# Optimization experiments

Measured on AMD Instinct MI355X. Metric: run time of the kernel, lower is better.

The kernel has to match this reference:

```python
import jax, jax.numpy as jnp
import numpy as np
from jax import lax

B, T, F = 8, 512, 128          # batch, mel time, mel freq
DM, DS, DC, EXP, NL = 384, 16, 4, 2, 12
DI = EXP * DM                   # 768 inner width
DTR = (DM + 15) // 16           # 24, mamba_ssm dt_rank='auto'
PT = PF = 16
L = (T // PT) * (F // PF)       # 256 patches
NC = 4


def setup_inputs() -> dict:
    key = jax.random.key(0)
    ks = iter(jax.random.split(key, 24))
    def n(shape, s=0.02):
        return jax.random.normal(next(ks), shape, jnp.float32) * s
    return {
        "x": jax.random.normal(next(ks), (B, T, F), jnp.float32),
        "patch_w": n((DM, PT, PF)),
        "patch_b": jnp.zeros((DM,), jnp.float32),
        "pos_embed": n((1, L, DM)),
        "ln_g": jnp.ones((NL, DM), jnp.float32),
        "ln_b": jnp.zeros((NL, DM), jnp.float32),
        "in_proj_w": n((NL, 2 * DI, DM)),
        "conv_w": n((NL, DI, DC), 0.1),
        "conv_b": jnp.zeros((NL, DI), jnp.float32),
        "x_proj_w": n((NL, DTR + 2 * DS, DI)),
        "dt_proj_w": n((NL, DI, DTR), 0.1),
        "dt_proj_b": n((NL, DI), 0.1),
        "A_log": jnp.tile(jnp.log(jnp.arange(1, DS + 1, dtype=jnp.float32))[None, None, :], (NL, DI, 1)),
        "Dskip": jnp.ones((NL, DI), jnp.float32),
        "out_proj_w": n((NL, DM, DI)),
        "fn_g": jnp.ones((DM,), jnp.float32),
        "fn_b": jnp.zeros((DM,), jnp.float32),
        "head_w": n((NC, DM)),
        "head_b": jnp.zeros((NC,), jnp.float32),
    }


def _layernorm(x, g, b):
    m = x.mean(-1, keepdims=True)
    v = jnp.var(x, axis=-1, keepdims=True)
    return (x - m) * lax.rsqrt(v + 1e-5) * g + b


def _silu(v):
    return v * jax.nn.sigmoid(v)


def _mamba_block(x, p):
    # x: [B, L, DM]; residual Mamba block (pre-LN, dropout=identity in eval)
    ln_g, ln_b, Wi, cw, cb, Wx, Wdt, bdt, A_log, Dsk, Wo = p
    res = x
    h = _layernorm(x, ln_g, ln_b)
    xz = jnp.einsum('bld,ed->ble', h, Wi)          # [B,L,2*DI]
    u, z = jnp.split(xz, 2, axis=-1)
    # causal depthwise conv1d, kernel DC (small, unrolled)
    up = jnp.pad(u, ((0, 0), (DC - 1, 0), (0, 0)))
    u = sum(up[:, k:k + L, :] * cw[:, k] for k in range(DC)) + cb
    u = _silu(u)
    proj = jnp.einsum('bld,ed->ble', u, Wx)        # [B,L,DTR+2*DS]
    dt, Bm, Cm = jnp.split(proj, [DTR, DTR + DS], axis=-1)
    delta = jax.nn.softplus(jnp.einsum('blr,dr->bld', dt, Wdt) + bdt)  # [B,L,DI]
    A = -jnp.exp(A_log)                            # [DI, DS]
    dA = jnp.exp(delta[..., None] * A)             # [B,L,DI,DS]
    dBu = (delta * u)[..., None] * Bm[:, :, None, :]

    def step(hst, inp):
        dA_t, dBu_t, C_t = inp
        hst = dA_t * hst + dBu_t                   # [B,DI,DS]
        return hst, jnp.einsum('bdn,bn->bd', hst, C_t)

    h0 = jnp.zeros((x.shape[0], DI, DS), x.dtype)
    _, ys = lax.scan(step, h0, (dA.swapaxes(0, 1), dBu.swapaxes(0, 1), Cm.swapaxes(0, 1)))
    y = ys.swapaxes(0, 1) + u * Dsk                # [B,L,DI]
    y = y * _silu(z)
    return res + jnp.einsum('bld,ed->ble', y, Wo)


def reference(x, patch_w, patch_b, pos_embed, ln_g, ln_b, in_proj_w, conv_w, conv_b,
              x_proj_w, dt_proj_w, dt_proj_b, A_log, Dskip, out_proj_w,
              fn_g, fn_b, head_w, head_b):
    Bn = x.shape[0]
    # patch embed = non-overlapping 16x16 conv == blocked reshape + einsum
    patches = x.reshape(Bn, T // PT, PT, F // PF, PF)
    tok = jnp.einsum('bhpwq,dpq->bhwd', patches, patch_w) + patch_b
    tok = tok.reshape(Bn, L, DM) + pos_embed

    def layer(carry, p):
        return _mamba_block(carry, p), None

    tok, _ = lax.scan(layer, tok, (ln_g, ln_b, in_proj_w, conv_w, conv_b,
                                   x_proj_w, dt_proj_w, dt_proj_b, A_log, Dskip, out_proj_w))
    tok = _layernorm(tok, fn_g, fn_b)
    pooled = tok.mean(axis=1)
    return pooled @ head_w.T + head_b
```

## Files before the change

### kernel.cpp

```cpp
#include <hip/hip_runtime.h>
#include <math.h>

namespace {

constexpr int kB   = 8;
constexpr int kL   = 256;
constexpr int kTok = 2048;
constexpr int kDM  = 384;
constexpr int kDI  = 768;
constexpr int kDS  = 16;
constexpr int kDTR = 24;
constexpr int kPROJ = 56;
constexpr int kNL  = 12;

constexpr int kWIN  = 2 * kDI * kDM;
constexpr int kWOUT = kDM * kDI;
constexpr int kWX   = kPROJ * kDI;
constexpr int kWTOT = kWIN + kWOUT + kWX;

typedef float f32x4 __attribute__((ext_vector_type(4)));
typedef short short8 __attribute__((ext_vector_type(8)));

__device__ __forceinline__ float softplus_f(float x) {
  return (x > 20.f) ? x : log1pf(__expf(x));
}
__device__ __forceinline__ float silu_f(float x) {
  return x / (1.f + __expf(-x));
}
__device__ __forceinline__ unsigned short f2bf(float f) {
  union { float f; unsigned u; } v; v.f = f;
  unsigned r = v.u + 0x7FFFu + ((v.u >> 16) & 1u);
  return (unsigned short)(r >> 16);
}

__global__ __launch_bounds__(256) void patch_gemm_k(
    const float* __restrict__ x, const float* __restrict__ Bw,
    const float* __restrict__ bias, const float* __restrict__ pos,
    float* __restrict__ C) {
  __shared__ float As[16][68];
  __shared__ float Bs[16][68];
  int tid = threadIdx.x;
  int bm = blockIdx.y * 64;
  int bn = blockIdx.x * 64;
  int lr = tid >> 2;
  int lk = (tid & 3) << 2;
  int tm = (tid >> 4) << 2;
  int tn = (tid & 15) << 2;
  float acc[4][4] = {};
  for (int k0 = 0; k0 < 256; k0 += 16) {
    {
      int token = bm + lr;
      int b = token >> 8, l = token & 255;
      int h = l >> 3, w = l & 7;
      int p = k0 >> 4;
      const float* ap = x + ((size_t)(b * 512) + h * 16 + p) * 128 + w * 16 + lk;
      float4 av = *(const float4*)ap;
      As[lk + 0][lr] = av.x; As[lk + 1][lr] = av.y;
      As[lk + 2][lr] = av.z; As[lk + 3][lr] = av.w;
    }
    {
      const float* bp = Bw + (size_t)(bn + lr) * 256 + k0 + lk;
      float4 bv = *(const float4*)bp;
      Bs[lk + 0][lr] = bv.x; Bs[lk + 1][lr] = bv.y;
      Bs[lk + 2][lr] = bv.z; Bs[lk + 3][lr] = bv.w;
    }
    __syncthreads();
    #pragma unroll
    for (int k = 0; k < 16; ++k) {
      float4 a = *(const float4*)&As[k][tm];
      float4 b = *(const float4*)&Bs[k][tn];
      float av[4] = {a.x, a.y, a.z, a.w};
      float bv[4] = {b.x, b.y, b.z, b.w};
      #pragma unroll
      for (int i = 0; i < 4; ++i)
        #pragma unroll
        for (int j = 0; j < 4; ++j)
          acc[i][j] = fmaf(av[i], bv[j], acc[i][j]);
    }
    __syncthreads();
  }
  #pragma unroll
  for (int i = 0; i < 4; ++i) {
    int row = bm + tm + i;
    #pragma unroll
    for (int j = 0; j < 4; ++j) {
      int col = bn + tn + j;
      C[(size_t)row * kDM + col] =
          acc[i][j] + bias[col] + pos[(size_t)(row & 255) * kDM + col];
    }
  }
}

template <bool BF16OUT>
__global__ __launch_bounds__(384) void ln_k(
    const float* __restrict__ in, void* __restrict__ outv,
    const float* __restrict__ g, const float* __restrict__ bb,
    float* __restrict__ proj_zero) {
  int t = blockIdx.x, d = threadIdx.x;
  if (proj_zero && d < kPROJ) proj_zero[(size_t)t * kPROJ + d] = 0.f;
  float v = in[(size_t)t * kDM + d];
  float s = v, s2 = v * v;
  #pragma unroll
  for (int m = 32; m >= 1; m >>= 1) {
    s  += __shfl_xor(s, m);
    s2 += __shfl_xor(s2, m);
  }
  __shared__ float ps[6], ps2[6];
  if ((d & 63) == 0) { ps[d >> 6] = s; ps2[d >> 6] = s2; }
  __syncthreads();
  float S = 0.f, S2 = 0.f;
  #pragma unroll
  for (int i = 0; i < 6; ++i) { S += ps[i]; S2 += ps2[i]; }
  float mean = S * (1.f / 384.f);
  float var  = S2 * (1.f / 384.f) - mean * mean;
  float r = rsqrtf(var + 1e-5f);
  float o = (v - mean) * r * g[d] + bb[d];
  if (BF16OUT) ((unsigned short*)outv)[(size_t)t * kDM + d] = f2bf(o);
  else ((float*)outv)[(size_t)t * kDM + d] = o;
}

__global__ __launch_bounds__(256) void convert_all_k(
    const float* __restrict__ w_in, const float* __restrict__ w_out,
    const float* __restrict__ w_x, unsigned short* __restrict__ dst) {
  int layer = blockIdx.y;
  int i4 = (blockIdx.x * 256 + threadIdx.x) * 4;
  if (i4 >= kWTOT) return;
  const float* src;
  int off;
  if (i4 < kWIN) { src = w_in + (size_t)layer * kWIN; off = i4; }
  else if (i4 < kWIN + kWOUT) { src = w_out + (size_t)layer * kWOUT; off = i4 - kWIN; }
  else { src = w_x + (size_t)layer * kWX; off = i4 - kWIN - kWOUT; }
  float4 v = *(const float4*)(src + off);
  unsigned short o[4] = {f2bf(v.x), f2bf(v.y), f2bf(v.z), f2bf(v.w)};
  *(uint2*)(dst + (size_t)layer * kWTOT + i4) = *(const uint2*)o;
}

template <int BN, int EPIL>
__global__ __launch_bounds__(256) void bgemm_k(
    const unsigned short* __restrict__ A, int lda,
    const unsigned short* __restrict__ B, int ldb,
    float* __restrict__ C, int ldc, int N, int Kc) {
  __shared__ __align__(16) unsigned short As[4][128][8];
  __shared__ __align__(16) unsigned short Bs[4][BN][8];
  int tid = threadIdx.x;
  int bm = blockIdx.y * 128;
  int bn = blockIdx.x * BN;
  int k_begin = blockIdx.z * Kc;
  int wave = tid >> 6, lane = tid & 63;
  int lm = lane & 15, lq = lane >> 4;
  int wm, wn;
  if (BN == 128) { wm = (wave >> 1) * 64; wn = (wave & 1) * 64; }
  else           { wm = wave * 32;        wn = 0; }
  constexpr int MT = (BN == 128) ? 4 : 2;
  f32x4 acc[MT][4] = {};

  for (int kt = 0; kt < Kc; kt += 32) {
    int k0 = k_begin + kt;
    int ar0 = tid & 127, aq0 = tid >> 7;
    int aq1 = aq0 + 2;
    uint4 a0 = *(const uint4*)(A + (size_t)(bm + ar0) * lda + k0 + aq0 * 8);
    uint4 a1 = *(const uint4*)(A + (size_t)(bm + ar0) * lda + k0 + aq1 * 8);
    uint4 b0, b1;
    int br0, bq0, br1 = 0, bq1 = 0;
    if (BN == 128) {
      br0 = tid & 127; bq0 = tid >> 7; br1 = br0; bq1 = bq0 + 2;
      b0 = *(const uint4*)(B + (size_t)(bn + br0) * ldb + k0 + bq0 * 8);
      b1 = *(const uint4*)(B + (size_t)(bn + br1) * ldb + k0 + bq1 * 8);
    } else {
      br0 = tid & 63; bq0 = tid >> 6;
      if (bn + br0 < N)
        b0 = *(const uint4*)(B + (size_t)(bn + br0) * ldb + k0 + bq0 * 8);
      else
        b0 = make_uint4(0u, 0u, 0u, 0u);
    }
    __syncthreads();
    *(uint4*)&As[aq0][ar0][0] = a0;
    *(uint4*)&As[aq1][ar0][0] = a1;
    *(uint4*)&Bs[bq0][br0][0] = b0;
    if (BN == 128) *(uint4*)&Bs[bq1][br1][0] = b1;
    __syncthreads();

    short8 bfrag[4];
    #pragma unroll
    for (int ni = 0; ni < 4; ++ni)
      bfrag[ni] = *(const short8*)&Bs[lq][wn + ni * 16 + lm][0];
    #pragma unroll
    for (int mi = 0; mi < MT; ++mi) {
      short8 afrag = *(const short8*)&As[lq][wm + mi * 16 + lm][0];
      #pragma unroll
      for (int ni = 0; ni < 4; ++ni)
        acc[mi][ni] = __builtin_amdgcn_mfma_f32_16x16x32_bf16(
            afrag, bfrag[ni], acc[mi][ni], 0, 0, 0);
    }
  }

  #pragma unroll
  for (int mi = 0; mi < MT; ++mi) {
    #pragma unroll
    for (int ni = 0; ni < 4; ++ni) {
      int grow0 = bm + wm + mi * 16 + lq * 4;
      int gcol = bn + wn + ni * 16 + lm;
      #pragma unroll
      for (int r = 0; r < 4; ++r) {
        float v = acc[mi][ni][r];
        int grow = grow0 + r;
        if (EPIL == 0) {
          C[(size_t)grow * ldc + gcol] = v;
        } else {
          if (gcol < N) atomicAdd(&C[(size_t)grow * ldc + gcol], v);
        }
      }
    }
  }
}

__global__ __launch_bounds__(256) void conv_tr_k(
    const float* __restrict__ xz, const float* __restrict__ cw,
    const float* __restrict__ cb, float* __restrict__ uT,
    float* __restrict__ sgT, unsigned short* __restrict__ u_bf) {
  int b = blockIdx.y;
  int l0 = blockIdx.x * 16;
  int tid = threadIdx.x;
  #pragma unroll
  for (int ch = 0; ch < 3; ++ch) {
    int d = ch * 256 + tid;
    float w0 = cw[d * 4], w1 = cw[d * 4 + 1], w2 = cw[d * 4 + 2], w3 = cw[d * 4 + 3];
    float bias = cb[d];
    float v[19];
    #pragma unroll
    for (int j = 0; j < 19; ++j) {
      int l = l0 - 3 + j;
      v[j] = (l >= 0) ? xz[(size_t)(b * kL + l) * (2 * kDI) + d] : 0.f;
    }
    float* up = uT + ((size_t)b * kDI + d) * kL + l0;
    float* sp = sgT + ((size_t)b * kDI + d) * kL + l0;
    #pragma unroll
    for (int i = 0; i < 16; ++i) {
      float acc = bias;
      acc = fmaf(v[i], w0, acc);
      acc = fmaf(v[i + 1], w1, acc);
      acc = fmaf(v[i + 2], w2, acc);
      acc = fmaf(v[i + 3], w3, acc);
      float o = silu_f(acc);
      up[i] = o;
      u_bf[(size_t)(b * kL + l0 + i) * kDI + d] = f2bf(o);
      float zv = xz[(size_t)(b * kL + l0 + i) * (2 * kDI) + kDI + d];
      sp[i] = silu_f(zv);
    }
  }
}

__global__ __launch_bounds__(128) void scanreg_k(
    const float* __restrict__ proj, const float* __restrict__ uT,
    const float* __restrict__ sgT, const float* __restrict__ dtw,
    const float* __restrict__ dtb, const float* __restrict__ A_log,
    const float* __restrict__ Dsk, unsigned short* __restrict__ y_bf) {
  int d0 = blockIdx.x * 8;
  int b = blockIdx.y;
  int tid = threadIdx.x;
  int c = tid >> 3;
  int dsub = tid & 7;
  int d = d0 + dsub;
  __shared__ float sh[16][8][20];
  __shared__ float sca[16][8][20];

  float Av[16];
  {
    const float* ap = A_log + (size_t)d * kDS;
    #pragma unroll
    for (int q = 0; q < 4; ++q) {
      float4 v = ((const float4*)ap)[q];
      Av[q * 4 + 0] = -__expf(v.x);
      Av[q * 4 + 1] = -__expf(v.y);
      Av[q * 4 + 2] = -__expf(v.z);
      Av[q * 4 + 3] = -__expf(v.w);
    }
  }
  float bdt = dtb[d];
  float Dv = Dsk[d];

  float u_[16];
  {
    const float* up = uT + ((size_t)b * kDI + d) * kL + c * 16;
    #pragma unroll
    for (int q = 0; q < 4; ++q) {
      float4 v = ((const float4*)up)[q];
      u_[q * 4 + 0] = v.x; u_[q * 4 + 1] = v.y;
      u_[q * 4 + 2] = v.z; u_[q * 4 + 3] = v.w;
    }
  }

  const float* pr = proj + ((size_t)(b * kL) + c * 16) * kPROJ;

  float dt_[16];
  {
    float wdt[24];
    const float* wp = dtw + (size_t)d * kDTR;
    #pragma unroll
    for (int q = 0; q < 6; ++q) {
      float4 v = ((const float4*)wp)[q];
      wdt[q * 4 + 0] = v.x; wdt[q * 4 + 1] = v.y;
      wdt[q * 4 + 2] = v.z; wdt[q * 4 + 3] = v.w;
    }
    #pragma unroll
    for (int i = 0; i < 16; ++i) {
      const float* p = pr + (size_t)i * kPROJ;
      float acc = bdt;
      #pragma unroll
      for (int q = 0; q < 6; ++q) {
        float4 v = ((const float4*)p)[q];
        acc = fmaf(v.x, wdt[q * 4 + 0], acc);
        acc = fmaf(v.y, wdt[q * 4 + 1], acc);
        acc = fmaf(v.z, wdt[q * 4 + 2], acc);
        acc = fmaf(v.w, wdt[q * 4 + 3], acc);
      }
      dt_[i] = softplus_f(acc);
    }
  }

  float h[16], ca[16];
  #pragma unroll
  for (int n = 0; n < 16; ++n) { h[n] = 0.f; ca[n] = 1.f; }
  #pragma unroll
  for (int i = 0; i < 16; ++i) {
    float dl = dt_[i];
    float du = dl * u_[i];
    const float* p = pr + (size_t)i * kPROJ + 24;
    float Bv[16];
    #pragma unroll
    for (int q = 0; q < 4; ++q) {
      float4 v = ((const float4*)p)[q];
      Bv[q * 4 + 0] = v.x; Bv[q * 4 + 1] = v.y;
      Bv[q * 4 + 2] = v.z; Bv[q * 4 + 3] = v.w;
    }
    #pragma unroll
    for (int n = 0; n < 16; ++n) {
      float a = __expf(dl * Av[n]);
      h[n] = fmaf(a, h[n], du * Bv[n]);
      ca[n] *= a;
    }
  }
  #pragma unroll
  for (int q = 0; q < 4; ++q) {
    *(float4*)&sh[c][dsub][q * 4] =
        make_float4(h[q * 4], h[q * 4 + 1], h[q * 4 + 2], h[q * 4 + 3]);
    *(float4*)&sca[c][dsub][q * 4] =
        make_float4(ca[q * 4], ca[q * 4 + 1], ca[q * 4 + 2], ca[q * 4 + 3]);
  }
  __syncthreads();

  float h0[16];
  #pragma unroll
  for (int n = 0; n < 16; ++n) h0[n] = 0.f;
  for (int j = 0; j < c; ++j) {
    #pragma unroll
    for (int q = 0; q < 4; ++q) {
      float4 hh = *(const float4*)&sh[j][dsub][q * 4];
      float4 aa = *(const float4*)&sca[j][dsub][q * 4];
      h0[q * 4 + 0] = fmaf(aa.x, h0[q * 4 + 0], hh.x);
      h0[q * 4 + 1] = fmaf(aa.y, h0[q * 4 + 1], hh.y);
      h0[q * 4 + 2] = fmaf(aa.z, h0[q * 4 + 2], hh.z);
      h0[q * 4 + 3] = fmaf(aa.w, h0[q * 4 + 3], hh.w);
    }
  }

  float sg_[16];
  {
    const float* sp = sgT + ((size_t)b * kDI + d) * kL + c * 16;
    #pragma unroll
    for (int q = 0; q < 4; ++q) {
      float4 v = ((const float4*)sp)[q];
      sg_[q * 4 + 0] = v.x; sg_[q * 4 + 1] = v.y;
      sg_[q * 4 + 2] = v.z; sg_[q * 4 + 3] = v.w;
    }
  }

  unsigned short* yp = y_bf + (size_t)(b * kL + c * 16) * kDI + d;
  #pragma unroll
  for (int i = 0; i < 16; ++i) {
    float dl = dt_[i];
    float du = dl * u_[i];
    const float* p = pr + (size_t)i * kPROJ + 24;
    float Bv[16], Cv[16];
    #pragma unroll
    for (int q = 0; q < 4; ++q) {
      float4 v = ((const float4*)p)[q];
      float4 w = ((const float4*)p)[q + 4];
      Bv[q * 4 + 0] = v.x; Bv[q * 4 + 1] = v.y;
      Bv[q * 4 + 2] = v.z; Bv[q * 4 + 3] = v.w;
      Cv[q * 4 + 0] = w.x; Cv[q * 4 + 1] = w.y;
      Cv[q * 4 + 2] = w.z; Cv[q * 4 + 3] = w.w;
    }
    float yv = 0.f;
    #pragma unroll
    for (int n = 0; n < 16; ++n) {
      float a = __expf(dl * Av[n]);
      h0[n] = fmaf(a, h0[n], du * Bv[n]);
      yv = fmaf(h0[n], Cv[n], yv);
    }
    yp[(size_t)i * kDI] = f2bf((yv + u_[i] * Dv) * sg_[i]);
  }
}

__global__ __launch_bounds__(384) void pool_k(
    const float* __restrict__ h, float* __restrict__ pooled) {
  int b = blockIdx.x, d = threadIdx.x;
  float acc = 0.f;
  for (int l = 0; l < kL; ++l) acc += h[(size_t)(b * kL + l) * kDM + d];
  pooled[b * kDM + d] = acc * (1.f / 256.f);
}

__global__ __launch_bounds__(64) void head_k(
    const float* __restrict__ pooled, const float* __restrict__ hw,
    const float* __restrict__ hb, float* __restrict__ out) {
  int b = blockIdx.x >> 2, c = blockIdx.x & 3;
  int lane = threadIdx.x;
  float acc = 0.f;
  for (int dd = lane; dd < kDM; dd += 64)
    acc = fmaf(pooled[b * kDM + dd], hw[c * kDM + dd], acc);
  #pragma unroll
  for (int m = 32; m >= 1; m >>= 1) acc += __shfl_xor(acc, m);
  if (lane == 0) out[b * 4 + c] = acc + hb[c];
}

}

extern "C" void kernel_launch(void* const* d_in, const int* in_sizes, int n_in,
                              void* d_out, int out_size, void* d_ws, size_t ws_size,
                              hipStream_t stream) {
  (void)in_sizes; (void)n_in; (void)out_size; (void)ws_size;
  const float* x        = (const float*)d_in[0];
  const float* patch_w  = (const float*)d_in[1];
  const float* patch_b  = (const float*)d_in[2];
  const float* pos      = (const float*)d_in[3];
  const float* ln_g     = (const float*)d_in[4];
  const float* ln_b     = (const float*)d_in[5];
  const float* in_w     = (const float*)d_in[6];
  const float* conv_w   = (const float*)d_in[7];
  const float* conv_b   = (const float*)d_in[8];
  const float* xproj_w  = (const float*)d_in[9];
  const float* dtproj_w = (const float*)d_in[10];
  const float* dtproj_b = (const float*)d_in[11];
  const float* A_log    = (const float*)d_in[12];
  const float* Dskip    = (const float*)d_in[13];
  const float* out_w    = (const float*)d_in[14];
  const float* fn_g     = (const float*)d_in[15];
  const float* fn_b     = (const float*)d_in[16];
  const float* head_w   = (const float*)d_in[17];
  const float* head_b   = (const float*)d_in[18];
  float* out = (float*)d_out;

  float* ws = (float*)d_ws;
  float* tok    = ws; ws += kTok * kDM;
  float* xz     = ws; ws += kTok * 2 * kDI;
  float* uT     = ws; ws += kTok * kDI;
  float* sgT    = ws; ws += kTok * kDI;
  float* proj   = ws; ws += kTok * kPROJ;
  float* pooled = ws; ws += kB * kDM;
  unsigned short* h_bf = (unsigned short*)ws; ws += kTok * kDM / 2;
  unsigned short* y_bf = (unsigned short*)ws; ws += kTok * kDI / 2;
  unsigned short* u_bf = (unsigned short*)ws; ws += kTok * kDI / 2;
  unsigned short* w_bf = (unsigned short*)ws; ws += (size_t)kNL * kWTOT / 2;
  float* lnout = xz;

  convert_all_k<<<dim3(kWTOT / 4 / 256, kNL), 256, 0, stream>>>(
      in_w, out_w, xproj_w, w_bf);

  patch_gemm_k<<<dim3(6, 32), 256, 0, stream>>>(x, patch_w, patch_b, pos, tok);

  for (int layer = 0; layer < kNL; ++layer) {
    const unsigned short* wl = w_bf + (size_t)layer * kWTOT;
    ln_k<true><<<kTok, kDM, 0, stream>>>(tok, h_bf, ln_g + layer * kDM,
                                         ln_b + layer * kDM, proj);
    bgemm_k<64, 0><<<dim3(24, 16, 1), 256, 0, stream>>>(
        h_bf, kDM, wl, kDM, xz, 2 * kDI, 2 * kDI, kDM);
    conv_tr_k<<<dim3(16, kB), 256, 0, stream>>>(
        xz, conv_w + layer * kDI * 4, conv_b + layer * kDI, uT, sgT, u_bf);
    bgemm_k<64, 1><<<dim3(1, 16, 6), 256, 0, stream>>>(
        u_bf, kDI, wl + kWIN + kWOUT, kDI, proj, kPROJ, kPROJ, kDI / 6);
    scanreg_k<<<dim3(kDI / 8, kB), 128, 0, stream>>>(
        proj, uT, sgT, dtproj_w + (size_t)layer * kDI * kDTR,
        dtproj_b + layer * kDI, A_log + (size_t)layer * kDI * kDS,
        Dskip + layer * kDI, y_bf);
    bgemm_k<128, 1><<<dim3(3, 16, 2), 256, 0, stream>>>(
        y_bf, kDI, wl + kWIN, kDI, tok, kDM, kDM, kDI / 2);
  }

  ln_k<false><<<kTok, kDM, 0, stream>>>(tok, lnout, fn_g, fn_b, nullptr);
  pool_k<<<kB, kDM, 0, stream>>>(lnout, pooled);
  head_k<<<kB * 4, 64, 0, stream>>>(pooled, head_w, head_b, out);
}
```

Baseline: 1.399 ms.

## Split scan state dimension across lane pairs and store xz/gate in bf16

The chunked selective-scan kernel now uses 256 threads per block. Each pair of lanes holds half of the 16 SSM states, and the two partial outputs are combined with a shuffle. Each lane computes half of the dt values and exchanges the rest, which lowers register pressure and raises parallelism. The in_proj GEMM now writes xz in bf16 and the silu(z) gate is stored in bf16, which cuts memory traffic in the conv and scan kernels at some cost in precision.

```diff
diff --git a/kernel.cpp b/kernel.cpp
--- a/kernel.cpp
+++ b/kernel.cpp
@@ -31,6 +31,9 @@
   union { float f; unsigned u; } v; v.f = f;
   unsigned r = v.u + 0x7FFFu + ((v.u >> 16) & 1u);
   return (unsigned short)(r >> 16);
+}
+__device__ __forceinline__ float bf2f(unsigned short u) {
+  return __uint_as_float((unsigned)u << 16);
 }
 
 __global__ __launch_bounds__(256) void patch_gemm_k(
@@ -139,7 +142,7 @@
 __global__ __launch_bounds__(256) void bgemm_k(
     const unsigned short* __restrict__ A, int lda,
     const unsigned short* __restrict__ B, int ldb,
-    float* __restrict__ C, int ldc, int N, int Kc) {
+    void* __restrict__ Cv, int ldc, int N, int Kc) {
   __shared__ __align__(16) unsigned short As[4][128][8];
   __shared__ __align__(16) unsigned short Bs[4][BN][8];
   int tid = threadIdx.x;
@@ -205,9 +208,11 @@
         float v = acc[mi][ni][r];
         int grow = grow0 + r;
         if (EPIL == 0) {
-          C[(size_t)grow * ldc + gcol] = v;
+          ((float*)Cv)[(size_t)grow * ldc + gcol] = v;
+        } else if (EPIL == 1) {
+          if (gcol < N) atomicAdd(&((float*)Cv)[(size_t)grow * ldc + gcol], v);
         } else {
-          if (gcol < N) atomicAdd(&C[(size_t)grow * ldc + gcol], v);
+          ((unsigned short*)Cv)[(size_t)grow * ldc + gcol] = f2bf(v);
         }
       }
     }
@@ -215,9 +220,9 @@
 }
 
 __global__ __launch_bounds__(256) void conv_tr_k(
-    const float* __restrict__ xz, const float* __restrict__ cw,
+    const unsigned short* __restrict__ xz, const float* __restrict__ cw,
     const float* __restrict__ cb, float* __restrict__ uT,
-    float* __restrict__ sgT, unsigned short* __restrict__ u_bf) {
+    unsigned short* __restrict__ sgT, unsigned short* __restrict__ u_bf) {
   int b = blockIdx.y;
   int l0 = blockIdx.x * 16;
   int tid = threadIdx.x;
@@ -230,10 +235,10 @@
     #pragma unroll
     for (int j = 0; j < 19; ++j) {
       int l = l0 - 3 + j;
-      v[j] = (l >= 0) ? xz[(size_t)(b * kL + l) * (2 * kDI) + d] : 0.f;
+      v[j] = (l >= 0) ? bf2f(xz[(size_t)(b * kL + l) * (2 * kDI) + d]) : 0.f;
     }
     float* up = uT + ((size_t)b * kDI + d) * kL + l0;
-    float* sp = sgT + ((size_t)b * kDI + d) * kL + l0;
+    unsigned short* sp = sgT + ((size_t)b * kDI + d) * kL + l0;
     #pragma unroll
     for (int i = 0; i < 16; ++i) {
       float acc = bias;
@@ -244,31 +249,32 @@
       float o = silu_f(acc);
       up[i] = o;
       u_bf[(size_t)(b * kL + l0 + i) * kDI + d] = f2bf(o);
-      float zv = xz[(size_t)(b * kL + l0 + i) * (2 * kDI) + kDI + d];
-      sp[i] = silu_f(zv);
-    }
-  }
-}
-
-__global__ __launch_bounds__(128) void scanreg_k(
+      float zv = bf2f(xz[(size_t)(b * kL + l0 + i) * (2 * kDI) + kDI + d]);
+      sp[i] = f2bf(silu_f(zv));
+    }
+  }
+}
+
+__global__ __launch_bounds__(256) void scansplit_k(
     const float* __restrict__ proj, const float* __restrict__ uT,
-    const float* __restrict__ sgT, const float* __restrict__ dtw,
+    const unsigned short* __restrict__ sgT, const float* __restrict__ dtw,
     const float* __restrict__ dtb, const float* __restrict__ A_log,
     const float* __restrict__ Dsk, unsigned short* __restrict__ y_bf) {
   int d0 = blockIdx.x * 8;
   int b = blockIdx.y;
   int tid = threadIdx.x;
-  int c = tid >> 3;
   int dsub = tid & 7;
+  int nh = (tid >> 3) & 1;
+  int c = tid >> 4;
   int d = d0 + dsub;
-  __shared__ float sh[16][8][20];
-  __shared__ float sca[16][8][20];
-
-  float Av[16];
-  {
-    const float* ap = A_log + (size_t)d * kDS;
-    #pragma unroll
-    for (int q = 0; q < 4; ++q) {
+  __shared__ float sh[16][16][9];
+  __shared__ float sca[16][16][9];
+
+  float Av[8];
+  {
+    const float* ap = A_log + (size_t)d * kDS + nh * 8;
+    #pragma unroll
+    for (int q = 0; q < 2; ++q) {
       float4 v = ((const float4*)ap)[q];
       Av[q * 4 + 0] = -__expf(v.x);
       Av[q * 4 + 1] = -__expf(v.y);
@@ -279,20 +285,9 @@
   float bdt = dtb[d];
   float Dv = Dsk[d];
 
-  float u_[16];
-  {
-    const float* up = uT + ((size_t)b * kDI + d) * kL + c * 16;
-    #pragma unroll
-    for (int q = 0; q < 4; ++q) {
-      float4 v = ((const float4*)up)[q];
-      u_[q * 4 + 0] = v.x; u_[q * 4 + 1] = v.y;
-      u_[q * 4 + 2] = v.z; u_[q * 4 + 3] = v.w;
-    }
-  }
-
   const float* pr = proj + ((size_t)(b * kL) + c * 16) * kPROJ;
 
-  float dt_[16];
+  float dtlo[8], dthi[8];
   {
     float wdt[24];
     const float* wp = dtw + (size_t)d * kDTR;
@@ -302,9 +297,11 @@
       wdt[q * 4 + 0] = v.x; wdt[q * 4 + 1] = v.y;
       wdt[q * 4 + 2] = v.z; wdt[q * 4 + 3] = v.w;
     }
-    #pragma unroll
-    for (int i = 0; i < 16; ++i) {
-      const float* p = pr + (size_t)i * kPROJ;
+    const float* prm = pr + (size_t)(nh * 8) * kPROJ;
+    float mine[8];
+    #pragma unroll
+    for (int i = 0; i < 8; ++i) {
+      const float* p = prm + (size_t)i * kPROJ;
       float acc = bdt;
       #pragma unroll
       for (int q = 0; q < 6; ++q) {
@@ -314,91 +311,95 @@
         acc = fmaf(v.z, wdt[q * 4 + 2], acc);
         acc = fmaf(v.w, wdt[q * 4 + 3], acc);
       }
-      dt_[i] = softplus_f(acc);
-    }
-  }
-
-  float h[16], ca[16];
-  #pragma unroll
-  for (int n = 0; n < 16; ++n) { h[n] = 0.f; ca[n] = 1.f; }
+      mine[i] = softplus_f(acc);
+    }
+    #pragma unroll
+    for (int i = 0; i < 8; ++i) {
+      float other = __shfl_xor(mine[i], 8);
+      dtlo[i] = nh ? other : mine[i];
+      dthi[i] = nh ? mine[i] : other;
+    }
+  }
+
+  float u_[16];
+  {
+    const float* up = uT + ((size_t)b * kDI + d) * kL + c * 16;
+    #pragma unroll
+    for (int q = 0; q < 4; ++q) {
+      float4 v = ((const float4*)up)[q];
+      u_[q * 4 + 0] = v.x; u_[q * 4 + 1] = v.y;
+      u_[q * 4 + 2] = v.z; u_[q * 4 + 3] = v.w;
+    }
+  }
+
+  float h[8], ca[8];
+  #pragma unroll
+  for (int n = 0; n < 8; ++n) { h[n] = 0.f; ca[n] = 1.f; }
   #pragma unroll
   for (int i = 0; i < 16; ++i) {
-    float dl = dt_[i];
+    float dl = (i < 8) ? dtlo[i] : dthi[i - 8];
     float du = dl * u_[i];
-    const float* p = pr + (size_t)i * kPROJ + 24;
-    float Bv[16];
-    #pragma unroll
-    for (int q = 0; q < 4; ++q) {
-      float4 v = ((const float4*)p)[q];
-      Bv[q * 4 + 0] = v.x; Bv[q * 4 + 1] = v.y;
-      Bv[q * 4 + 2] = v.z; Bv[q * 4 + 3] = v.w;
-    }
-    #pragma unroll
-    for (int n = 0; n < 16; ++n) {
+    const float* p = pr + (size_t)i * kPROJ + 24 + nh * 8;
+    float4 b0 = ((const float4*)p)[0];
+    float4 b1 = ((const float4*)p)[1];
+    float Bv[8] = {b0.x, b0.y, b0.z, b0.w, b1.x, b1.y, b1.z, b1.w};
+    #pragma unroll
+    for (int n = 0; n < 8; ++n) {
       float a = __expf(dl * Av[n]);
       h[n] = fmaf(a, h[n], du * Bv[n]);
       ca[n] *= a;
     }
   }
-  #pragma unroll
-  for (int q = 0; q < 4; ++q) {
-    *(float4*)&sh[c][dsub][q * 4] =
-        make_float4(h[q * 4], h[q * 4 + 1], h[q * 4 + 2], h[q * 4 + 3]);
-    *(float4*)&sca[c][dsub][q * 4] =
-        make_float4(ca[q * 4], ca[q * 4 + 1], ca[q * 4 + 2], ca[q * 4 + 3]);
+  {
+    int nrow = nh * 8;
+    #pragma unroll
+    for (int q = 0; q < 8; ++q) {
+      sh[c][nrow + q][dsub] = h[q];
+      sca[c][nrow + q][dsub] = ca[q];
+    }
   }
   __syncthreads();
 
-  float h0[16];
-  #pragma unroll
-  for (int n = 0; n < 16; ++n) h0[n] = 0.f;
-  for (int j = 0; j < c; ++j) {
-    #pragma unroll
-    for (int q = 0; q < 4; ++q) {
-      float4 hh = *(const float4*)&sh[j][dsub][q * 4];
-      float4 aa = *(const float4*)&sca[j][dsub][q * 4];
-      h0[q * 4 + 0] = fmaf(aa.x, h0[q * 4 + 0], hh.x);
-      h0[q * 4 + 1] = fmaf(aa.y, h0[q * 4 + 1], hh.y);
-      h0[q * 4 + 2] = fmaf(aa.z, h0[q * 4 + 2], hh.z);
-      h0[q * 4 + 3] = fmaf(aa.w, h0[q * 4 + 3], hh.w);
+  float h0[8];
+  #pragma unroll
+  for (int n = 0; n < 8; ++n) h0[n] = 0.f;
+  {
+    int nrow = nh * 8;
+    for (int j = 0; j < c; ++j) {
+      #pragma unroll
+      for (int q = 0; q < 8; ++q)
+        h0[q] = fmaf(sca[j][nrow + q][dsub], h0[q], sh[j][nrow + q][dsub]);
     }
   }
 
   float sg_[16];
   {
-    const float* sp = sgT + ((size_t)b * kDI + d) * kL + c * 16;
-    #pragma unroll
-    for (int q = 0; q < 4; ++q) {
-      float4 v = ((const float4*)sp)[q];
-      sg_[q * 4 + 0] = v.x; sg_[q * 4 + 1] = v.y;
-      sg_[q * 4 + 2] = v.z; sg_[q * 4 + 3] = v.w;
-    }
+    const unsigned short* sp = sgT + ((size_t)b * kDI + d) * kL + c * 16;
+    #pragma unroll
+    for (int i = 0; i < 16; ++i) sg_[i] = bf2f(sp[i]);
   }
 
   unsigned short* yp = y_bf + (size_t)(b * kL + c * 16) * kDI + d;
   #pragma unroll
   for (int i = 0; i < 16; ++i) {
-    float dl = dt_[i];
+    float dl = (i < 8) ? dtlo[i] : dthi[i - 8];
     float du = dl * u_[i];
-    const float* p = pr + (size_t)i * kPROJ + 24;
-    float Bv[16], Cv[16];
-    #pragma unroll
-    for (int q = 0; q < 4; ++q) {
-      float4 v = ((const float4*)p)[q];
-      float4 w = ((const float4*)p)[q + 4];
-      Bv[q * 4 + 0] = v.x; Bv[q * 4 + 1] = v.y;
-      Bv[q * 4 + 2] = v.z; Bv[q * 4 + 3] = v.w;
-      Cv[q * 4 + 0] = w.x; Cv[q * 4 + 1] = w.y;
-      Cv[q * 4 + 2] = w.z; Cv[q * 4 + 3] = w.w;
-    }
+    const float* p = pr + (size_t)i * kPROJ + 24 + nh * 8;
+    float4 b0 = ((const float4*)p)[0];
+    float4 b1 = ((const float4*)p)[1];
+    float4 c0 = ((const float4*)(p + 16))[0];
+    float4 c1 = ((const float4*)(p + 16))[1];
+    float Bv[8] = {b0.x, b0.y, b0.z, b0.w, b1.x, b1.y, b1.z, b1.w};
+    float Cv[8] = {c0.x, c0.y, c0.z, c0.w, c1.x, c1.y, c1.z, c1.w};
     float yv = 0.f;
     #pragma unroll
-    for (int n = 0; n < 16; ++n) {
+    for (int n = 0; n < 8; ++n) {
       float a = __expf(dl * Av[n]);
       h0[n] = fmaf(a, h0[n], du * Bv[n]);
       yv = fmaf(h0[n], Cv[n], yv);
     }
-    yp[(size_t)i * kDI] = f2bf((yv + u_[i] * Dv) * sg_[i]);
+    yv += __shfl_xor(yv, 8);
+    if (nh == 0) yp[(size_t)i * kDI] = f2bf((yv + u_[i] * Dv) * sg_[i]);
   }
 }
 
@@ -452,16 +453,16 @@
 
   float* ws = (float*)d_ws;
   float* tok    = ws; ws += kTok * kDM;
-  float* xz     = ws; ws += kTok * 2 * kDI;
   float* uT     = ws; ws += kTok * kDI;
-  float* sgT    = ws; ws += kTok * kDI;
   float* proj   = ws; ws += kTok * kPROJ;
   float* pooled = ws; ws += kB * kDM;
-  unsigned short* h_bf = (unsigned short*)ws; ws += kTok * kDM / 2;
-  unsigned short* y_bf = (unsigned short*)ws; ws += kTok * kDI / 2;
-  unsigned short* u_bf = (unsigned short*)ws; ws += kTok * kDI / 2;
-  unsigned short* w_bf = (unsigned short*)ws; ws += (size_t)kNL * kWTOT / 2;
-  float* lnout = xz;
+  unsigned short* xz_bf = (unsigned short*)ws; ws += kTok * 2 * kDI / 2;
+  unsigned short* sgT   = (unsigned short*)ws; ws += kTok * kDI / 2;
+  unsigned short* h_bf  = (unsigned short*)ws; ws += kTok * kDM / 2;
+  unsigned short* y_bf  = (unsigned short*)ws; ws += kTok * kDI / 2;
+  unsigned short* u_bf  = (unsigned short*)ws; ws += kTok * kDI / 2;
+  unsigned short* w_bf  = (unsigned short*)ws; ws += (size_t)kNL * kWTOT / 2;
+  float* lnout = uT;
 
   convert_all_k<<<dim3(kWTOT / 4 / 256, kNL), 256, 0, stream>>>(
       in_w, out_w, xproj_w, w_bf);
@@ -472,13 +473,13 @@
     const unsigned short* wl = w_bf + (size_t)layer * kWTOT;
     ln_k<true><<<kTok, kDM, 0, stream>>>(tok, h_bf, ln_g + layer * kDM,
                                          ln_b + layer * kDM, proj);
-    bgemm_k<64, 0><<<dim3(24, 16, 1), 256, 0, stream>>>(
-        h_bf, kDM, wl, kDM, xz, 2 * kDI, 2 * kDI, kDM);
+    bgemm_k<64, 3><<<dim3(24, 16, 1), 256, 0, stream>>>(
+        h_bf, kDM, wl, kDM, xz_bf, 2 * kDI, 2 * kDI, kDM);
     conv_tr_k<<<dim3(16, kB), 256, 0, stream>>>(
-        xz, conv_w + layer * kDI * 4, conv_b + layer * kDI, uT, sgT, u_bf);
+        xz_bf, conv_w + layer * kDI * 4, conv_b + layer * kDI, uT, sgT, u_bf);
     bgemm_k<64, 1><<<dim3(1, 16, 6), 256, 0, stream>>>(
         u_bf, kDI, wl + kWIN + kWOUT, kDI, proj, kPROJ, kPROJ, kDI / 6);
-    scanreg_k<<<dim3(kDI / 8, kB), 128, 0, stream>>>(
+    scansplit_k<<<dim3(kDI / 8, kB), 256, 0, stream>>>(
         proj, uT, sgT, dtproj_w + (size_t)layer * kDI * kDTR,
         dtproj_b + layer * kDI, A_log + (size_t)layer * kDI * kDS,
         Dskip + layer * kDI, y_bf);
```

Result: faster. 1.344 ms (-3.9%).
